# Optimization experiments

Measured on AMD Instinct MI355X. Metric: run time of the kernel, lower is better.

## Reference

```python
import jax, jax.numpy as jnp
import numpy as np
from jax import lax

DN2 = ('NCHW', 'OIHW', 'NCHW')
DN3 = ('NCDHW', 'OIDHW', 'NCDHW')


def _convlstm_step(h, c, x, W, b):
    # x: [B, Cin, H, W], h/c: [B, nf, H, W], W: [4*nf, Cin+nf, 3, 3]
    comb = jnp.concatenate([x, h], axis=1)
    cc = lax.conv_general_dilated(comb, W, (1, 1), 'SAME', dimension_numbers=DN2)
    cc = cc + b[None, :, None, None]
    ci, cf, co, cg = jnp.split(cc, 4, axis=1)
    i = jax.nn.sigmoid(ci)
    f = jax.nn.sigmoid(cf)
    o = jax.nn.sigmoid(co)
    g = jnp.tanh(cg)
    c_next = f * c + i * g
    h_next = o * jnp.tanh(c_next)
    return h_next, c_next


def setup_inputs() -> dict:
    key = jax.random.key(0)
    ks = jax.random.split(key, 4)
    B, T, Cin, H, W = 32, 12, 1, 64, 64
    nf = 64
    s = 0.05
    return {
        'x': jax.random.normal(ks[0], (B, T, Cin, H, W), jnp.float32),
        'future_step': 12,
        'W_enc': jax.random.normal(ks[1], (4 * nf, Cin + nf, 3, 3), jnp.float32) * s,
        'b_enc': jnp.zeros((4 * nf,), jnp.float32),
        'W_dec': jax.random.normal(ks[2], (4 * nf, nf + nf, 3, 3), jnp.float32) * s,
        'b_dec': jnp.zeros((4 * nf,), jnp.float32),
        'W_cnn': jax.random.normal(ks[3], (1, nf, 1, 3, 3), jnp.float32) * s,
        'b_cnn': jnp.zeros((1,), jnp.float32),
    }


def reference(x, future_step, W_enc, b_enc, W_dec, b_dec, W_cnn, b_cnn):
    B, T, Cin, H, Wd = x.shape
    nf = W_enc.shape[0] // 4
    h0 = jnp.zeros((B, nf, H, Wd), x.dtype)
    c0 = jnp.zeros((B, nf, H, Wd), x.dtype)

    # ---- encoder: scan over time ----
    def enc_step(carry, xt):
        h, c = carry
        h, c = _convlstm_step(h, c, xt, W_enc, b_enc)
        return (h, c), None

    (h_t, _), _ = lax.scan(enc_step, (h0, c0), jnp.moveaxis(x, 1, 0))
    encoder_vector = h_t
    out_encoder_vector = encoder_vector.reshape(B, -1)

    # ---- decoder: feed back h as next input ----
    def dec_step(carry, _):
        ev, h, c = carry
        h, c = _convlstm_step(h, c, ev, W_dec, b_dec)
        return (h, h, c), h

    _, outs = lax.scan(dec_step, (encoder_vector, h0, c0), None, length=future_step)
    # outs: [Tf, B, nf, H, W] -> [B, nf, Tf, H, W]
    outs = jnp.transpose(outs, (1, 2, 0, 3, 4))

    # ---- 3D CNN head: kernel (1,3,3), padding (0,1,1) ----
    y = lax.conv_general_dilated(outs, W_cnn, (1, 1, 1),
                                 [(0, 0), (1, 1), (1, 1)],
                                 dimension_numbers=DN3)
    y = y + b_cnn[None, :, None, None, None]
    # [B, 1, Tf, H, W] -> [B, Tf, 1, H, W]
    y = jnp.transpose(y, (0, 2, 1, 3, 4))
    return y, out_encoder_vector
```

## Files before the change

### kernel.cpp

```cpp
#include <hip/hip_runtime.h>
#include <hip/hip_bf16.h>


#define HW 4096
#define NF 64

typedef __attribute__((ext_vector_type(8))) short bf16x8;
typedef __attribute__((ext_vector_type(4))) float f32x4;

__device__ __forceinline__ float fsig(float v) {
  return __builtin_amdgcn_rcpf(1.f + __expf(-v));
}
__device__ __forceinline__ float ftanh(float v) {
  float vc = fminf(fmaxf(v, -15.f), 15.f);
  float e = __expf(2.f * vc);
  return (e - 1.f) * __builtin_amdgcn_rcpf(e + 1.f);
}
__device__ __forceinline__ float bf2f(short s) {
  union { unsigned u; float f; } a;
  a.u = ((unsigned)(unsigned short)s) << 16;
  return a.f;
}
__device__ __forceinline__ short f2bf(float f) {
  union { float f; unsigned u; } a;
  a.f = f;
  unsigned r = (a.u + 0x7fff + ((a.u >> 16) & 1)) >> 16;
  return (short)r;
}
__device__ __forceinline__ void dma16(const short* g, short* l) {
  __builtin_amdgcn_global_load_lds(
      (const __attribute__((address_space(1))) char*)g,
      (__attribute__((address_space(3))) char*)l, 16, 0, 0);
}

template <bool HAS_X>
__global__ __launch_bounds__(512) void lstm_mfma_k(
    const short* __restrict__ hin,
    const short* __restrict__ W,
    const float* __restrict__ wx,
    const float* __restrict__ xpl,
    const float* __restrict__ bias,
    const float* __restrict__ cin,
    const short* __restrict__ zbuf,
    short* __restrict__ hout,
    float* __restrict__ cout) {
  const int b = blockIdx.x;
  const int y = blockIdx.y;
  const int tid = threadIdx.x;
  const int lane = tid & 63;
  const int wv = tid >> 6;
  const int wnf = wv & 3;
  const int whalf = wv >> 2;
  const int col = lane & 15;
  const int quad = lane >> 4;

  __shared__ short As3[3][8192];
  __shared__ short Bs[3 * 66 * 64];
  __shared__ float xs[3][64];

  const short* hb = hin + (size_t)b * (HW * 64);
#pragma unroll
  for (int r = 0; r < 3; ++r) {
    const int py = y - 1 + r;
    const short* src = (py >= 0 && py < 64)
        ? hb + ((py * 64 + 8 * wv + (lane >> 3)) * 64 + (lane & 7) * 8)
        : zbuf + lane * 8;
    dma16(src, &Bs[(r * 66 + 8 * wv + 1) * 64]);
  }
#pragma unroll
  for (int k = 0; k < 2; ++k) {
    const short* src = W + (k >> 1) * 16384 + (k & 1) * 8192;
    dma16(src + (wv * 64 + lane) * 8, &As3[k][wv * 64 * 8]);
    dma16(src + (512 + wv * 64 + lane) * 8, &As3[k][(512 + wv * 64) * 8]);
  }
  if (tid < 48) {
    const int r = tid >> 4;
    const int s = ((tid >> 3) & 1) * 65;
    const int ch0 = (tid & 7) * 8;
    bf16x8 z = {0, 0, 0, 0, 0, 0, 0, 0};
    *reinterpret_cast<bf16x8*>(&Bs[(r * 66 + s) * 64 + ch0]) = z;
  }
  if (HAS_X) {
    if (tid < 192) {
      const float* xb = xpl + (size_t)b * (12 * HW);
      const int r = tid >> 6, cx = tid & 63;
      const int py = y - 1 + r;
      xs[r][cx] = (py >= 0 && py < 64) ? xb[py * 64 + cx] : 0.f;
    }
  }
  asm volatile("s_waitcnt vmcnt(2) lgkmcnt(0)" ::: "memory");
  __builtin_amdgcn_s_barrier();

  f32x4 acc[4][2];
#pragma unroll
  for (int g = 0; g < 4; ++g) {
    const int oc0 = g * 64 + wnf * 16 + quad * 4;
#pragma unroll
    for (int nt = 0; nt < 2; ++nt)
#pragma unroll
      for (int r = 0; r < 4; ++r) acc[g][nt][r] = bias[oc0 + r];
  }

  if (HAS_X) {
#pragma unroll
    for (int nt = 0; nt < 2; ++nt) {
      const int px = whalf * 32 + nt * 16 + col;
#pragma unroll
      for (int tap = 0; tap < 9; ++tap) {
        const int pxx = px + (tap % 3) - 1;
        const float xv = (pxx >= 0 && pxx < 64) ? xs[tap / 3][pxx] : 0.f;
#pragma unroll
        for (int g = 0; g < 4; ++g) {
          const int oc0 = g * 64 + wnf * 16 + quad * 4;
#pragma unroll
          for (int r = 0; r < 4; ++r)
            acc[g][nt][r] = fmaf(xv, wx[(oc0 + r) * 9 + tap], acc[g][nt][r]);
        }
      }
    }
  }

  const int axr = (col & 7) << 3;
#pragma unroll
  for (int k = 0; k < 18; ++k) {
    const int tap = k >> 1, gp = k & 1, p = k % 3;
    if (k > 0) {
      if (k == 17)
        asm volatile("s_waitcnt vmcnt(0)" ::: "memory");
      else
        asm volatile("s_waitcnt vmcnt(2)" ::: "memory");
      __builtin_amdgcn_s_barrier();
    }
    if (k + 2 < 18) {
      const int nk = k + 2;
      const short* src = W + (nk >> 1) * 16384 + (nk & 1) * 8192;
      dma16(src + (wv * 64 + lane) * 8, &As3[nk % 3][wv * 64 * 8]);
      dma16(src + (512 + wv * 64 + lane) * 8, &As3[nk % 3][(512 + wv * 64) * 8]);
    }
    const int hr = tap / 3;
    const int sb = col + tap % 3;
    const int sx = (sb & 7) << 3;
    const int srow = (hr * 66 + whalf * 32 + sb) * 64;
#pragma unroll
    for (int kc = 0; kc < 2; ++kc) {
      const int chb = kc * 32 + quad * 8;
      const int abase = ((wnf * 16 + col) * 64 + chb) ^ axr;
      const int bbase = (srow + chb) ^ sx;
      bf16x8 a0 = *reinterpret_cast<const bf16x8*>(&As3[p][abase]);
      bf16x8 a1 = *reinterpret_cast<const bf16x8*>(&As3[p][abase + 4096]);
      bf16x8 b0 = *reinterpret_cast<const bf16x8*>(&Bs[bbase]);
      bf16x8 b1 = *reinterpret_cast<const bf16x8*>(&Bs[bbase + 1024]);
      __builtin_amdgcn_s_setprio(1);
      acc[gp * 2][0] = __builtin_amdgcn_mfma_f32_16x16x32_bf16(a0, b0, acc[gp * 2][0], 0, 0, 0);
      acc[gp * 2][1] = __builtin_amdgcn_mfma_f32_16x16x32_bf16(a0, b1, acc[gp * 2][1], 0, 0, 0);
      acc[gp * 2 + 1][0] = __builtin_amdgcn_mfma_f32_16x16x32_bf16(a1, b0, acc[gp * 2 + 1][0], 0, 0, 0);
      acc[gp * 2 + 1][1] = __builtin_amdgcn_mfma_f32_16x16x32_bf16(a1, b1, acc[gp * 2 + 1][1], 0, 0, 0);
      __builtin_amdgcn_s_setprio(0);
    }
  }

  const int nf0 = wnf * 16 + quad * 4;
#pragma unroll
  for (int nt = 0; nt < 2; ++nt) {
    const int px = whalf * 32 + nt * 16 + col;
    const int swz = ((px + 1) & 7) << 3;
    const size_t pix = (size_t)b * HW + y * 64 + px;
    f32x4 cold = *reinterpret_cast<const f32x4*>(cin + pix * 64 + nf0);
    f32x4 cnew;
    short hnew[4];
#pragma unroll
    for (int r = 0; r < 4; ++r) {
      float i_ = fsig(acc[0][nt][r]);
      float f_ = fsig(acc[1][nt][r]);
      float o_ = fsig(acc[2][nt][r]);
      float g_ = ftanh(acc[3][nt][r]);
      float cn = fmaf(f_, cold[r], i_ * g_);
      cnew[r] = cn;
      hnew[r] = f2bf(o_ * ftanh(cn));
    }
    *reinterpret_cast<f32x4*>(cout + pix * 64 + nf0) = cnew;
    short4 hv = make_short4(hnew[0], hnew[1], hnew[2], hnew[3]);
    *reinterpret_cast<short4*>(hout + pix * 64 + (nf0 ^ swz)) = hv;
  }
}

__global__ __launch_bounds__(256) void head_k(const short* __restrict__ h,
                                              const float* __restrict__ wc2,
                                              const float* __restrict__ bc,
                                              float* __restrict__ yout, int t) {
  const int tid = blockIdx.x * 256 + threadIdx.x;
  const int pix = tid & 4095;
  const int b = tid >> 12;
  const int x0 = pix & 63, y0 = pix >> 6;
  float acc = bc[0];
  const short* hb = h + (size_t)b * (HW * 64);
#pragma unroll
  for (int tap = 0; tap < 9; ++tap) {
    const int yy = y0 + tap / 3 - 1, xx = x0 + (tap % 3) - 1;
    if (yy < 0 || yy > 63 || xx < 0 || xx > 63) continue;
    const short* hp = hb + (yy * 64 + xx) * 64;
    const int sw8 = (xx + 1) & 7;
    const float* wp = wc2 + tap * 64;
#pragma unroll
    for (int f8 = 0; f8 < 8; ++f8) {
      bf16x8 v = *reinterpret_cast<const bf16x8*>(hp + ((f8 ^ sw8) * 8));
#pragma unroll
      for (int j = 0; j < 8; ++j) acc = fmaf(wp[f8 * 8 + j], bf2f(v[j]), acc);
    }
  }
  yout[(size_t)(b * 12 + t) * HW + pix] = acc;
}

__global__ __launch_bounds__(256) void ev_out_k(const short* __restrict__ h,
                                                float* __restrict__ out) {
  __shared__ float tl[64][65];
  const int b = blockIdx.y, pg = blockIdx.x;
  const int p0 = pg * 64;
  {
    const int pixl = threadIdx.x >> 2, c0 = (threadIdx.x & 3) * 16;
    const int sw8 = (pixl + 1) & 7;
    const short* hp = h + ((size_t)b * HW + p0 + pixl) * 64;
#pragma unroll
    for (int gi = 0; gi < 2; ++gi) {
      const int grp = (c0 >> 3) + gi;
      bf16x8 v = *reinterpret_cast<const bf16x8*>(hp + ((grp ^ sw8) * 8));
#pragma unroll
      for (int j = 0; j < 8; ++j) tl[pixl][grp * 8 + j] = bf2f(v[j]);
    }
  }
  __syncthreads();
  {
    const int ch = threadIdx.x >> 2, q0 = (threadIdx.x & 3) * 16;
    float* op = out + ((size_t)b * 64 + ch) * (size_t)HW + p0 + q0;
#pragma unroll
    for (int i = 0; i < 16; ++i) op[i] = tl[q0 + i][ch];
  }
}

__global__ __launch_bounds__(256) void reo_enc_k(const float* __restrict__ src,
                                                 short* __restrict__ Wh,
                                                 float* __restrict__ wx) {
  const int idx = blockIdx.x * 256 + threadIdx.x;
  if (idx < 9 * 256 * 64) {
    const int tap = idx >> 14, oc = (idx >> 6) & 255, c = idx & 63;
    const int dst = tap * 16384 + (((oc * 64) + c) ^ ((oc & 7) << 3));
    Wh[dst] = f2bf(src[(oc * 65 + (c + 1)) * 9 + tap]);
  }
  if (idx < 256 * 9) {
    const int oc = idx / 9, tap = idx % 9;
    wx[idx] = src[(oc * 65 + 0) * 9 + tap];
  }
}

__global__ __launch_bounds__(256) void reo_dec_k(const float* __restrict__ src,
                                                 short* __restrict__ Wx,
                                                 short* __restrict__ Ws) {
  const int idx = blockIdx.x * 256 + threadIdx.x;
  if (idx >= 9 * 256 * 64) return;
  const int tap = idx >> 14, oc = (idx >> 6) & 255, c = idx & 63;
  const int dst = tap * 16384 + (((oc * 64) + c) ^ ((oc & 7) << 3));
  const float a = src[(oc * 128 + c) * 9 + tap];
  const float b = src[(oc * 128 + 64 + c) * 9 + tap];
  Wx[dst] = f2bf(a);
  Ws[dst] = f2bf(a + b);
}

__global__ __launch_bounds__(256) void reo_cnn_k(const float* __restrict__ src,
                                                 float* __restrict__ wc2) {
  const int idx = blockIdx.x * 256 + threadIdx.x;
  if (idx >= 576) return;
  wc2[idx] = src[(idx % 64) * 9 + (idx / 64)];
}

extern "C" void kernel_launch(void* const* d_in, const int* in_sizes, int n_in,
                              void* d_out, int out_size, void* d_ws, size_t ws_size,
                              hipStream_t stream) {
  const float* x = (const float*)d_in[0];
  const float* W_enc = (const float*)d_in[2];
  const float* b_enc = (const float*)d_in[3];
  const float* W_dec = (const float*)d_in[4];
  const float* b_dec = (const float*)d_in[5];
  const float* W_cnn = (const float*)d_in[6];
  const float* b_cnn = (const float*)d_in[7];
  float* out = (float*)d_out;
  float* out_y = out;
  float* out_ev = out + 1572864;

  float* ws = (float*)d_ws;
  float* cA = ws;
  float* cB = cA + 8388608;
  short* hA = (short*)(cB + 8388608);
  short* hB = hA + 8388608;
  short* WEh = hB + 8388608;
  short* WDx = WEh + 147456;
  short* WDs = WDx + 147456;
  float* wx = (float*)(WDs + 147456);
  float* wc2 = wx + 2304;
  short* zb = (short*)(wc2 + 576);

  reo_enc_k<<<(147456 + 255) / 256, 256, 0, stream>>>(W_enc, WEh, wx);
  reo_dec_k<<<(147456 + 255) / 256, 256, 0, stream>>>(W_dec, WDx, WDs);
  reo_cnn_k<<<3, 256, 0, stream>>>(W_cnn, wc2);

  hipMemsetAsync(hA, 0, 8388608 * sizeof(short), stream);
  hipMemsetAsync(cA, 0, 8388608 * sizeof(float), stream);
  hipMemsetAsync(zb, 0, 512 * sizeof(short), stream);

  dim3 gridL(32, 64), blkL(512);
  dim3 gridE(64, 32), blkE(256);
  short *ha = hA, *hb = hB;
  float *ca = cA, *cb = cB;

  for (int t = 0; t < 12; ++t) {
    lstm_mfma_k<true><<<gridL, blkL, 0, stream>>>(ha, WEh, wx, x + t * HW,
                                                  b_enc, ca, zb, hb, cb);
    { short* tm = ha; ha = hb; hb = tm; }
    { float* tm = ca; ca = cb; cb = tm; }
  }
  ev_out_k<<<gridE, blkE, 0, stream>>>(ha, out_ev);

  hipMemsetAsync(cb, 0, 8388608 * sizeof(float), stream);
  { float* tm = ca; ca = cb; cb = tm; }

  for (int t = 0; t < 12; ++t) {
    lstm_mfma_k<false><<<gridL, blkL, 0, stream>>>(
        ha, (t == 0) ? WDx : WDs, nullptr, nullptr, b_dec, ca, zb, hb, cb);
    { short* tm = ha; ha = hb; hb = tm; }
    { float* tm = ca; ca = cb; cb = tm; }
    head_k<<<512, 256, 0, stream>>>(ha, wc2, b_cnn, out_y, t);
  }
}
```

Before: 1.940 ms.

## Fuse CNN head into decoder LSTM launches and skip zero-state work

The 3D CNN head for step t-1 now runs inside the decoder LSTM launch for step t, using extra blocks appended to the grid, so the separate head launches disappear except for the last one. The first encoder step is specialised to skip the h-convolution entirely, and the first steps of both phases skip reading c, which removes the h/c memsets. It also hoists the B-fragment LDS loads so each tap loads them once instead of per gate pair, and transposes wx so the x-conv can load weights as float4. In exchange, the fused head blocks compete with LSTM blocks for CUs within each launch.

```diff
diff --git a/kernel.cpp b/kernel.cpp
--- a/kernel.cpp
+++ b/kernel.cpp
@@ -33,7 +33,7 @@
       (__attribute__((address_space(3))) char*)l, 16, 0, 0);
 }
 
-template <bool HAS_X>
+template <bool HAS_X, bool HAS_H, bool FUSE_HEAD>
 __global__ __launch_bounds__(512) void lstm_mfma_k(
     const short* __restrict__ hin,
     const short* __restrict__ W,
@@ -43,7 +43,38 @@
     const float* __restrict__ cin,
     const short* __restrict__ zbuf,
     short* __restrict__ hout,
-    float* __restrict__ cout) {
+    float* __restrict__ cout,
+    const float* __restrict__ wc2,
+    const float* __restrict__ bcnn,
+    float* __restrict__ yout,
+    int th) {
+  if (FUSE_HEAD) {
+    if (blockIdx.x >= 32) {
+      const int f = ((blockIdx.x - 32) * 64 + blockIdx.y) * 512 + threadIdx.x;
+      const int pix = f & 4095;
+      const int b = f >> 12;
+      const int x0 = pix & 63, y0 = pix >> 6;
+      float acc = bcnn[0];
+      const short* hb = hin + (size_t)b * (HW * 64);
+#pragma unroll
+      for (int tap = 0; tap < 9; ++tap) {
+        const int yy = y0 + tap / 3 - 1, xx = x0 + (tap % 3) - 1;
+        if (yy < 0 || yy > 63 || xx < 0 || xx > 63) continue;
+        const short* hp = hb + (yy * 64 + xx) * 64;
+        const int sw8 = (xx + 1) & 7;
+        const float* wp = wc2 + tap * 64;
+#pragma unroll
+        for (int f8 = 0; f8 < 8; ++f8) {
+          bf16x8 v = *reinterpret_cast<const bf16x8*>(hp + ((f8 ^ sw8) * 8));
+#pragma unroll
+          for (int j = 0; j < 8; ++j)
+            acc = fmaf(wp[f8 * 8 + j], bf2f(v[j]), acc);
+        }
+      }
+      yout[(size_t)(b * 12 + th) * HW + pix] = acc;
+      return;
+    }
+  }
   const int b = blockIdx.x;
   const int y = blockIdx.y;
   const int tid = threadIdx.x;
@@ -58,27 +89,29 @@
   __shared__ short Bs[3 * 66 * 64];
   __shared__ float xs[3][64];
 
-  const short* hb = hin + (size_t)b * (HW * 64);
-#pragma unroll
-  for (int r = 0; r < 3; ++r) {
-    const int py = y - 1 + r;
-    const short* src = (py >= 0 && py < 64)
-        ? hb + ((py * 64 + 8 * wv + (lane >> 3)) * 64 + (lane & 7) * 8)
-        : zbuf + lane * 8;
-    dma16(src, &Bs[(r * 66 + 8 * wv + 1) * 64]);
-  }
-#pragma unroll
-  for (int k = 0; k < 2; ++k) {
-    const short* src = W + (k >> 1) * 16384 + (k & 1) * 8192;
-    dma16(src + (wv * 64 + lane) * 8, &As3[k][wv * 64 * 8]);
-    dma16(src + (512 + wv * 64 + lane) * 8, &As3[k][(512 + wv * 64) * 8]);
-  }
-  if (tid < 48) {
-    const int r = tid >> 4;
-    const int s = ((tid >> 3) & 1) * 65;
-    const int ch0 = (tid & 7) * 8;
-    bf16x8 z = {0, 0, 0, 0, 0, 0, 0, 0};
-    *reinterpret_cast<bf16x8*>(&Bs[(r * 66 + s) * 64 + ch0]) = z;
+  if (HAS_H) {
+    const short* hb = hin + (size_t)b * (HW * 64);
+#pragma unroll
+    for (int r = 0; r < 3; ++r) {
+      const int py = y - 1 + r;
+      const short* src = (py >= 0 && py < 64)
+          ? hb + ((py * 64 + 8 * wv + (lane >> 3)) * 64 + (lane & 7) * 8)
+          : zbuf + lane * 8;
+      dma16(src, &Bs[(r * 66 + 8 * wv + 1) * 64]);
+    }
+#pragma unroll
+    for (int k = 0; k < 2; ++k) {
+      const short* src = W + (k >> 1) * 16384 + (k & 1) * 8192;
+      dma16(src + (wv * 64 + lane) * 8, &As3[k][wv * 64 * 8]);
+      dma16(src + (512 + wv * 64 + lane) * 8, &As3[k][(512 + wv * 64) * 8]);
+    }
+    if (tid < 48) {
+      const int r = tid >> 4;
+      const int s = ((tid >> 3) & 1) * 65;
+      const int ch0 = (tid & 7) * 8;
+      bf16x8 z = {0, 0, 0, 0, 0, 0, 0, 0};
+      *reinterpret_cast<bf16x8*>(&Bs[(r * 66 + s) * 64 + ch0]) = z;
+    }
   }
   if (HAS_X) {
     if (tid < 192) {
@@ -88,8 +121,12 @@
       xs[r][cx] = (py >= 0 && py < 64) ? xb[py * 64 + cx] : 0.f;
     }
   }
-  asm volatile("s_waitcnt vmcnt(2) lgkmcnt(0)" ::: "memory");
-  __builtin_amdgcn_s_barrier();
+  if (HAS_H) {
+    asm volatile("s_waitcnt vmcnt(2) lgkmcnt(0)" ::: "memory");
+    __builtin_amdgcn_s_barrier();
+  } else {
+    __syncthreads();
+  }
 
   f32x4 acc[4][2];
 #pragma unroll
@@ -103,59 +140,74 @@
 
   if (HAS_X) {
 #pragma unroll
-    for (int nt = 0; nt < 2; ++nt) {
-      const int px = whalf * 32 + nt * 16 + col;
-#pragma unroll
-      for (int tap = 0; tap < 9; ++tap) {
-        const int pxx = px + (tap % 3) - 1;
-        const float xv = (pxx >= 0 && pxx < 64) ? xs[tap / 3][pxx] : 0.f;
-#pragma unroll
-        for (int g = 0; g < 4; ++g) {
-          const int oc0 = g * 64 + wnf * 16 + quad * 4;
+    for (int tap = 0; tap < 9; ++tap) {
+      float xv[2];
+#pragma unroll
+      for (int nt = 0; nt < 2; ++nt) {
+        const int pxx = whalf * 32 + nt * 16 + col + (tap % 3) - 1;
+        xv[nt] = (pxx >= 0 && pxx < 64) ? xs[tap / 3][pxx] : 0.f;
+      }
+      const float* wt = wx + tap * 256;
+#pragma unroll
+      for (int g = 0; g < 4; ++g) {
+        const int oc0 = g * 64 + wnf * 16 + quad * 4;
+        const f32x4 w4 = *reinterpret_cast<const f32x4*>(wt + oc0);
+#pragma unroll
+        for (int nt = 0; nt < 2; ++nt)
 #pragma unroll
           for (int r = 0; r < 4; ++r)
-            acc[g][nt][r] = fmaf(xv, wx[(oc0 + r) * 9 + tap], acc[g][nt][r]);
-        }
-      }
-    }
-  }
-
-  const int axr = (col & 7) << 3;
-#pragma unroll
-  for (int k = 0; k < 18; ++k) {
-    const int tap = k >> 1, gp = k & 1, p = k % 3;
-    if (k > 0) {
-      if (k == 17)
-        asm volatile("s_waitcnt vmcnt(0)" ::: "memory");
-      else
-        asm volatile("s_waitcnt vmcnt(2)" ::: "memory");
-      __builtin_amdgcn_s_barrier();
-    }
-    if (k + 2 < 18) {
-      const int nk = k + 2;
-      const short* src = W + (nk >> 1) * 16384 + (nk & 1) * 8192;
-      dma16(src + (wv * 64 + lane) * 8, &As3[nk % 3][wv * 64 * 8]);
-      dma16(src + (512 + wv * 64 + lane) * 8, &As3[nk % 3][(512 + wv * 64) * 8]);
-    }
-    const int hr = tap / 3;
-    const int sb = col + tap % 3;
-    const int sx = (sb & 7) << 3;
-    const int srow = (hr * 66 + whalf * 32 + sb) * 64;
-#pragma unroll
-    for (int kc = 0; kc < 2; ++kc) {
-      const int chb = kc * 32 + quad * 8;
-      const int abase = ((wnf * 16 + col) * 64 + chb) ^ axr;
-      const int bbase = (srow + chb) ^ sx;
-      bf16x8 a0 = *reinterpret_cast<const bf16x8*>(&As3[p][abase]);
-      bf16x8 a1 = *reinterpret_cast<const bf16x8*>(&As3[p][abase + 4096]);
-      bf16x8 b0 = *reinterpret_cast<const bf16x8*>(&Bs[bbase]);
-      bf16x8 b1 = *reinterpret_cast<const bf16x8*>(&Bs[bbase + 1024]);
-      __builtin_amdgcn_s_setprio(1);
-      acc[gp * 2][0] = __builtin_amdgcn_mfma_f32_16x16x32_bf16(a0, b0, acc[gp * 2][0], 0, 0, 0);
-      acc[gp * 2][1] = __builtin_amdgcn_mfma_f32_16x16x32_bf16(a0, b1, acc[gp * 2][1], 0, 0, 0);
-      acc[gp * 2 + 1][0] = __builtin_amdgcn_mfma_f32_16x16x32_bf16(a1, b0, acc[gp * 2 + 1][0], 0, 0, 0);
-      acc[gp * 2 + 1][1] = __builtin_amdgcn_mfma_f32_16x16x32_bf16(a1, b1, acc[gp * 2 + 1][1], 0, 0, 0);
-      __builtin_amdgcn_s_setprio(0);
+            acc[g][nt][r] = fmaf(xv[nt], w4[r], acc[g][nt][r]);
+      }
+    }
+  }
+
+  if (HAS_H) {
+    const int axr = (col & 7) << 3;
+    bf16x8 bh00, bh01, bh10, bh11;
+#pragma unroll
+    for (int k = 0; k < 18; ++k) {
+      const int tap = k >> 1, gp = k & 1, p = k % 3;
+      if (k > 0) {
+        if (k == 17)
+          asm volatile("s_waitcnt vmcnt(0)" ::: "memory");
+        else
+          asm volatile("s_waitcnt vmcnt(2)" ::: "memory");
+        __builtin_amdgcn_s_barrier();
+      }
+      if (k + 2 < 18) {
+        const int nk = k + 2;
+        const short* src = W + (nk >> 1) * 16384 + (nk & 1) * 8192;
+        dma16(src + (wv * 64 + lane) * 8, &As3[nk % 3][wv * 64 * 8]);
+        dma16(src + (512 + wv * 64 + lane) * 8,
+              &As3[nk % 3][(512 + wv * 64) * 8]);
+      }
+      if (gp == 0) {
+        const int hr = tap / 3;
+        const int sb = col + tap % 3;
+        const int sx = (sb & 7) << 3;
+        const int srow = (hr * 66 + whalf * 32 + sb) * 64;
+        const int b0 = (srow + quad * 8) ^ sx;
+        const int b1 = (srow + 32 + quad * 8) ^ sx;
+        bh00 = *reinterpret_cast<const bf16x8*>(&Bs[b0]);
+        bh01 = *reinterpret_cast<const bf16x8*>(&Bs[b0 + 1024]);
+        bh10 = *reinterpret_cast<const bf16x8*>(&Bs[b1]);
+        bh11 = *reinterpret_cast<const bf16x8*>(&Bs[b1 + 1024]);
+      }
+#pragma unroll
+      for (int kc = 0; kc < 2; ++kc) {
+        const int chb = kc * 32 + quad * 8;
+        const int abase = ((wnf * 16 + col) * 64 + chb) ^ axr;
+        bf16x8 a0 = *reinterpret_cast<const bf16x8*>(&As3[p][abase]);
+        bf16x8 a1 = *reinterpret_cast<const bf16x8*>(&As3[p][abase + 4096]);
+        const bf16x8 bb0 = kc ? bh10 : bh00;
+        const bf16x8 bb1 = kc ? bh11 : bh01;
+        __builtin_amdgcn_s_setprio(1);
+        acc[gp * 2][0] = __builtin_amdgcn_mfma_f32_16x16x32_bf16(a0, bb0, acc[gp * 2][0], 0, 0, 0);
+        acc[gp * 2][1] = __builtin_amdgcn_mfma_f32_16x16x32_bf16(a0, bb1, acc[gp * 2][1], 0, 0, 0);
+        acc[gp * 2 + 1][0] = __builtin_amdgcn_mfma_f32_16x16x32_bf16(a1, bb0, acc[gp * 2 + 1][0], 0, 0, 0);
+        acc[gp * 2 + 1][1] = __builtin_amdgcn_mfma_f32_16x16x32_bf16(a1, bb1, acc[gp * 2 + 1][1], 0, 0, 0);
+        __builtin_amdgcn_s_setprio(0);
+      }
     }
   }
 
@@ -165,7 +217,8 @@
     const int px = whalf * 32 + nt * 16 + col;
     const int swz = ((px + 1) & 7) << 3;
     const size_t pix = (size_t)b * HW + y * 64 + px;
-    f32x4 cold = *reinterpret_cast<const f32x4*>(cin + pix * 64 + nf0);
+    f32x4 cold = {0.f, 0.f, 0.f, 0.f};
+    if (cin) cold = *reinterpret_cast<const f32x4*>(cin + pix * 64 + nf0);
     f32x4 cnew;
     short hnew[4];
 #pragma unroll
@@ -247,7 +300,7 @@
     Wh[dst] = f2bf(src[(oc * 65 + (c + 1)) * 9 + tap]);
   }
   if (idx < 256 * 9) {
-    const int oc = idx / 9, tap = idx % 9;
+    const int tap = idx >> 8, oc = idx & 255;
     wx[idx] = src[(oc * 65 + 0) * 9 + tap];
   }
 }
@@ -301,32 +354,39 @@
   reo_enc_k<<<(147456 + 255) / 256, 256, 0, stream>>>(W_enc, WEh, wx);
   reo_dec_k<<<(147456 + 255) / 256, 256, 0, stream>>>(W_dec, WDx, WDs);
   reo_cnn_k<<<3, 256, 0, stream>>>(W_cnn, wc2);
-
-  hipMemsetAsync(hA, 0, 8388608 * sizeof(short), stream);
-  hipMemsetAsync(cA, 0, 8388608 * sizeof(float), stream);
   hipMemsetAsync(zb, 0, 512 * sizeof(short), stream);
 
   dim3 gridL(32, 64), blkL(512);
+  dim3 gridF(36, 64);
   dim3 gridE(64, 32), blkE(256);
-  short *ha = hA, *hb = hB;
-  float *ca = cA, *cb = cB;
-
-  for (int t = 0; t < 12; ++t) {
-    lstm_mfma_k<true><<<gridL, blkL, 0, stream>>>(ha, WEh, wx, x + t * HW,
-                                                  b_enc, ca, zb, hb, cb);
+
+  lstm_mfma_k<true, false, false><<<gridL, blkL, 0, stream>>>(
+      nullptr, WEh, wx, x, b_enc, nullptr, zb, hB, cB,
+      nullptr, nullptr, nullptr, 0);
+  short *ha = hB, *hb = hA;
+  float *ca = cB, *cb = cA;
+
+  for (int t = 1; t < 12; ++t) {
+    lstm_mfma_k<true, true, false><<<gridL, blkL, 0, stream>>>(
+        ha, WEh, wx, x + t * HW, b_enc, ca, zb, hb, cb,
+        nullptr, nullptr, nullptr, 0);
     { short* tm = ha; ha = hb; hb = tm; }
     { float* tm = ca; ca = cb; cb = tm; }
   }
   ev_out_k<<<gridE, blkE, 0, stream>>>(ha, out_ev);
 
-  hipMemsetAsync(cb, 0, 8388608 * sizeof(float), stream);
+  lstm_mfma_k<false, true, false><<<gridL, blkL, 0, stream>>>(
+      ha, WDx, nullptr, nullptr, b_dec, nullptr, zb, hb, cb,
+      nullptr, nullptr, nullptr, 0);
+  { short* tm = ha; ha = hb; hb = tm; }
   { float* tm = ca; ca = cb; cb = tm; }
 
-  for (int t = 0; t < 12; ++t) {
-    lstm_mfma_k<false><<<gridL, blkL, 0, stream>>>(
-        ha, (t == 0) ? WDx : WDs, nullptr, nullptr, b_dec, ca, zb, hb, cb);
+  for (int t = 1; t < 12; ++t) {
+    lstm_mfma_k<false, true, true><<<gridF, blkL, 0, stream>>>(
+        ha, WDs, nullptr, nullptr, b_dec, ca, zb, hb, cb,
+        wc2, b_cnn, out_y, t - 1);
     { short* tm = ha; ha = hb; hb = tm; }
     { float* tm = ca; ca = cb; cb = tm; }
-    head_k<<<512, 256, 0, stream>>>(ha, wc2, b_cnn, out_y, t);
-  }
-}
+  }
+  head_k<<<512, 256, 0, stream>>>(ha, wc2, b_cnn, out_y, 11);
+}
```

Result: faster. 1.815 ms (-6.4%).
